# Kernel tuning notes

Measured on AMD Instinct MI355X. Metric: run time of the kernel, lower is better.

Reference implementation:

```python
import jax, jax.numpy as jnp
import numpy as np
import math

B, S, H, NH, DK, K = 256, 200, 768, 12, 64, 64
EPS = 1e-12

def setup_inputs() -> dict:
    key = jax.random.key(0)
    ks = jax.random.split(key, 8)
    sc = 0.02
    return {
        "x": jax.random.normal(ks[0], (B, S, H), dtype=jnp.float32),
        "mask": jnp.ones((B, 1, S), dtype=jnp.float32),
        "Wq": jax.random.normal(ks[1], (H, H), dtype=jnp.float32) * sc,
        "bq": jnp.zeros((H,), dtype=jnp.float32),
        "Wk": jax.random.normal(ks[2], (H, H), dtype=jnp.float32) * sc,
        "bk": jnp.zeros((H,), dtype=jnp.float32),
        "Wv": jax.random.normal(ks[3], (H, H), dtype=jnp.float32) * sc,
        "bv": jnp.zeros((H,), dtype=jnp.float32),
        "We": jax.random.normal(ks[4], (K, S), dtype=jnp.float32) * sc,
        "be": jnp.zeros((K,), dtype=jnp.float32),
        "Wf": jax.random.normal(ks[5], (K, S), dtype=jnp.float32) * sc,
        "bf": jnp.zeros((K,), dtype=jnp.float32),
        "Wd": jax.random.normal(ks[6], (H, H), dtype=jnp.float32) * sc,
        "bd": jnp.zeros((H,), dtype=jnp.float32),
        "gamma": jnp.ones((H,), dtype=jnp.float32),
        "beta": jnp.zeros((H,), dtype=jnp.float32),
    }

def _heads(t):  # [B,S,H] -> [B,NH,S,DK]
    return t.reshape(B, S, NH, DK).transpose(0, 2, 1, 3)

def reference(x, mask, Wq, bq, Wk, bk, Wv, bv, We, be, Wf, bf, Wd, bd, gamma, beta):
    q = _heads(x @ Wq.T + bq)
    k = _heads(x @ Wk.T + bk)
    v = _heads(x @ Wv.T + bv)
    m = mask[:, 0:1, :, None]            # [B,1,S,1]
    k = k * m
    v = v * m
    # Linformer seq projections: E on value, F on key (applied along seq axis)
    v = jnp.einsum("bhsd,ks->bhkd", v, We) + be[:, None]   # [B,NH,K,DK]
    k = jnp.einsum("bhsd,ks->bhkd", k, Wf) + bf[:, None]   # [B,NH,K,DK]
    scores = jnp.einsum("bhqd,bhkd->bhqk", q, k) / math.sqrt(DK)
    p_attn = jax.nn.softmax(scores, axis=-1)               # [B,NH,S,K]
    ctx = jnp.einsum("bhqk,bhkd->bhqd", p_attn, v)         # [B,NH,S,DK]
    ctx = ctx.transpose(0, 2, 1, 3).reshape(B, S, H)
    h = ctx @ Wd.T + bd + x                                # dense + residual (dropout=0)
    mu = jnp.mean(h, axis=-1, keepdims=True)
    var = jnp.mean(jnp.square(h - mu), axis=-1, keepdims=True)
    out = (h - mu) / jnp.sqrt(var + EPS) * gamma + beta
    return out, p_attn
```

## Files before the change

kernel.cpp:

```cpp
#include <hip/hip_runtime.h>
#include <stdint.h>

typedef unsigned short u16;
typedef short bf16x8 __attribute__((ext_vector_type(8)));
typedef float f32x4 __attribute__((ext_vector_type(4)));
typedef unsigned short u16x4 __attribute__((ext_vector_type(4)));

#define NB   256
#define NS   200
#define NHID 768
#define NHEAD 12
#define NDK  64
#define NK   64
#define NBH  (NB*NHEAD)
#define NM   (NB*NS)

__device__ __forceinline__ u16 f2b(float f){
  unsigned u = __builtin_bit_cast(unsigned, f);
  return (u16)((u + 0x7FFFu + ((u>>16)&1u)) >> 16);
}
__device__ __forceinline__ float b2f(u16 b){
  return __builtin_bit_cast(float, (unsigned)b << 16);
}
__device__ __forceinline__ bf16x8 pack8(const float* v){
  bf16x8 r;
#pragma unroll
  for (int i=0;i<8;i++) r[i] = (short)f2b(v[i]);
  return r;
}
__device__ __forceinline__ f32x4 mfma16(bf16x8 a, bf16x8 b, f32x4 c){
  return __builtin_amdgcn_mfma_f32_16x16x32_bf16(a, b, c, 0, 0, 0);
}
__device__ __forceinline__ void gload16(u16* l, const u16* g){
  __builtin_amdgcn_global_load_lds(
      (const __attribute__((address_space(1))) void*)g,
      (__attribute__((address_space(3))) void*)l, 16, 0, 0);
}

__global__ __launch_bounds__(256) void prep_kernel(
    const float* __restrict__ Wq, const float* __restrict__ Wk,
    const float* __restrict__ Wv, const float* __restrict__ Wd,
    const float* __restrict__ Wf, const float* __restrict__ We,
    const float* __restrict__ mask,
    u16* __restrict__ Wqb, u16* __restrict__ Wkb,
    u16* __restrict__ Wvb, u16* __restrict__ Wdb,
    u16* __restrict__ Wfeb, float* __restrict__ rs)
{
  const int blk = blockIdx.x, t = threadIdx.x;
  const int i = blk*256 + t;
  Wqb[i]=f2b(Wq[i]); Wkb[i]=f2b(Wk[i]); Wvb[i]=f2b(Wv[i]); Wdb[i]=f2b(Wd[i]);
  if (blk < 128){
    float v = 0.f;
    if (t < NS) v = (blk<64) ? Wf[blk*NS+t] : We[(blk-64)*NS+t];
    Wfeb[blk*256+t] = f2b(v);
  }
  if (blk >= 1024 && blk < 1280 && t < 128){
    const int b = blk-1024;
    const float* src = (t<64) ? (Wf + t*NS) : (We + (t-64)*NS);
    float acc = 0.f;
    for (int s=0;s<NS;s++) acc += src[s]*mask[b*NS+s];
    rs[b*128+t] = acc;
  }
}

__global__ __launch_bounds__(256) void gemm_yfe2(
    const float* __restrict__ x, const float* __restrict__ mask,
    const u16* __restrict__ Wfeb, u16* __restrict__ yfe,
    u16* __restrict__ xb)
{
  __shared__ u16 Al[128*64];
  __shared__ u16 Bl[128*72];
  __shared__ float Ml[256];
  const int t=threadIdx.x, w=t>>6, lane=t&63, hi=lane>>4, lo=lane&15;
  const int sr=lane>>3, sc=lane&7;
  const int b=blockIdx.x, col0=blockIdx.y*128;
  const int a16 = t&15, q4 = t>>4;
  const int ss0 = q4*4;
  const int swzw = (a16&7)<<3;

  Ml[t] = (t<NS) ? mask[b*NS+t] : 0.f;

  f32x4 acc[4][4];
#pragma unroll
  for(int i=0;i<4;i++)
#pragma unroll
    for(int j=0;j<4;j++) acc[i][j]=(f32x4)0.0f;

  const u16* Ab=&Al[((w>>1)*64+lo)*64 + hi*8];
  int nb_[4], sw_[4];
#pragma unroll
  for (int j=0;j<4;j++){
    const int n = (w&1)*64 + j*16 + lo;
    nb_[j] = n*72;
    sw_[j] = ((n>>3)&7)<<3;
  }
  __syncthreads();

  for (int kt=0; kt<256; kt+=64){
#pragma unroll
    for (int i8=0;i8<4;i8++){
      const int r = w*32 + i8*8 + sr;
      gload16(&Al[r*64 + sc*8], Wfeb + (size_t)r*256 + kt + sc*8);
    }
    float vv[4][8];
#pragma unroll
    for (int ii=0;ii<4;ii++){
      const int s = kt + ss0 + ii;
      const int srow = (s<NS) ? s : (NS-1);
      const float* gp = x + ((size_t)b*NS + srow)*NHID + col0 + a16*8;
      float4 u0 = *(const float4*)gp, u1 = *(const float4*)(gp+4);
      if (s < NS){
        float tu[8] = {u0.x,u0.y,u0.z,u0.w,u1.x,u1.y,u1.z,u1.w};
        *(bf16x8*)(xb + ((size_t)b*NS + s)*NHID + col0 + a16*8) = pack8(tu);
      }
      const float m = Ml[s];
      vv[ii][0]=u0.x*m; vv[ii][1]=u0.y*m; vv[ii][2]=u0.z*m; vv[ii][3]=u0.w*m;
      vv[ii][4]=u1.x*m; vv[ii][5]=u1.y*m; vv[ii][6]=u1.z*m; vv[ii][7]=u1.w*m;
    }
    const int ss_swz = ss0 ^ swzw;
#pragma unroll
    for (int h=0;h<8;h++){
      u16x4 p;
      p[0]=f2b(vv[0][h]); p[1]=f2b(vv[1][h]);
      p[2]=f2b(vv[2][h]); p[3]=f2b(vv[3][h]);
      *(u16x4*)&Bl[(a16*8+h)*72 + ss_swz] = p;
    }
    asm volatile("s_waitcnt vmcnt(0)" ::: "memory");
    __syncthreads();
#pragma unroll
    for (int ks=0; ks<2; ks++){
      bf16x8 a[4], bfr[4];
#pragma unroll
      for (int i=0;i<4;i++) a[i]   = *(const bf16x8*)(Ab + i*16*64 + ks*32);
#pragma unroll
      for (int j=0;j<4;j++){
        const int s8 = ks*32 + hi*8;
        bfr[j] = *(const bf16x8*)&Bl[nb_[j] + (s8 ^ sw_[j])];
      }
#pragma unroll
      for (int i=0;i<4;i++)
#pragma unroll
        for (int j=0;j<4;j++) acc[i][j] = mfma16(a[i], bfr[j], acc[i][j]);
    }
    __syncthreads();
  }
  const int mbase=(w>>1)*64, nbase=col0+(w&1)*64;
#pragma unroll
  for (int i=0;i<4;i++)
#pragma unroll
    for (int r=0;r<4;r++){
      const int m = mbase + i*16 + hi*4 + r;
#pragma unroll
      for (int j=0;j<4;j++){
        const int n = nbase + j*16 + lo;
        yfe[(size_t)b*98304 + (size_t)m*NHID + n] = f2b(acc[i][j][r]);
      }
    }
}

template<int EPI>
__global__ __launch_bounds__(512, 2) void gemm_ring(
    const u16* __restrict__ Ag_, const u16* __restrict__ Bg_,
    const float* __restrict__ bias, const u16* __restrict__ resid,
    u16* __restrict__ Cout)
{
  __shared__ u16 AS[4][8192];
  __shared__ u16 BS[4][8192];
  const int t = threadIdx.x;
  const int w = t>>6, lane = t&63, hi = lane>>4, lo = lane&15;
  const int wm = w>>2, wn = w&3;
  const int bid = blockIdx.x;
  const int row0 = ((bid/24)*8 + (bid&7))*256;
  const int col0 = ((bid>>3)%3)*256;
  const u16* Ag = Ag_ + (size_t)row0*NHID;
  const u16* Bg = Bg_ + (size_t)col0*NHID;
  const int rp0 = t>>3, cc = t&7;

  f32x4 acc[8][4];
#pragma unroll
  for (int i=0;i<8;i++)
#pragma unroll
    for (int j=0;j<4;j++) acc[i][j] = (f32x4)0.0f;

  int aoff[8], boff[4];
#pragma unroll
  for (int i=0;i<8;i++){
    const int r = wm*128 + i*16 + lo;
    const int rp = r>>1, c = (r&1)*4 + hi;
    aoff[i] = rp*64 + ((c ^ (rp&7))<<3);
  }
#pragma unroll
  for (int j=0;j<4;j++){
    const int n = wn*64 + j*16 + lo;
    const int rp = n>>1, c = (n&1)*4 + hi;
    boff[j] = rp*64 + ((c ^ (rp&7))<<3);
  }

  auto stage = [&](int s, int kt){
#pragma unroll
    for (int i8=0;i8<2;i8++){
      const int rp = i8*64 + rp0;
      const int c  = cc ^ (rp&7);
      const int grow = rp*2 + (c>>2);
      const int gcol = (c&3)<<3;
      gload16(&AS[s][rp*64 + cc*8], Ag + (size_t)grow*NHID + kt + gcol);
      gload16(&BS[s][rp*64 + cc*8], Bg + (size_t)grow*NHID + kt + gcol);
    }
  };
  auto body = [&](const u16* as_, const u16* bs_){
    bf16x8 av[8], bvv[4];
#pragma unroll
    for (int j=0;j<4;j++) bvv[j] = *(const bf16x8*)(bs_ + boff[j]);
#pragma unroll
    for (int i=0;i<8;i++) av[i] = *(const bf16x8*)(as_ + aoff[i]);
    __builtin_amdgcn_s_setprio(1);
#pragma unroll
    for (int i=0;i<8;i++)
#pragma unroll
      for (int j=0;j<4;j++) acc[i][j] = mfma16(av[i], bvv[j], acc[i][j]);
    __builtin_amdgcn_s_setprio(0);
  };
  auto step = [&](int tt, int s){
    if (tt+3 < 24) stage((s+3)&3, (tt+3)*32);
    body(AS[s], BS[s]);
    if (tt <= 20)      { asm volatile("s_waitcnt vmcnt(8)" ::: "memory"); }
    else if (tt == 21) { asm volatile("s_waitcnt vmcnt(4)" ::: "memory"); }
    else if (tt == 22) { asm volatile("s_waitcnt vmcnt(0)" ::: "memory"); }
    if (tt < 23){
      __builtin_amdgcn_sched_barrier(0);
      asm volatile("s_barrier" ::: "memory");
      __builtin_amdgcn_sched_barrier(0);
    }
  };

  stage(0,0); stage(1,32); stage(2,64);
  asm volatile("s_waitcnt vmcnt(8)" ::: "memory");
  asm volatile("s_barrier" ::: "memory");
  __builtin_amdgcn_sched_barrier(0);

#pragma unroll
  for (int tt=0; tt<24; tt+=4){
    step(tt,0); step(tt+1,1); step(tt+2,2); step(tt+3,3);
  }

#pragma unroll
  for (int i=0;i<8;i++)
#pragma unroll
    for (int q=0;q<4;q++){
      const int m = row0 + wm*128 + i*16 + hi*4 + q;
#pragma unroll
      for (int j=0;j<4;j++){
        const int n = col0 + wn*64 + j*16 + lo;
        float v = acc[i][j][q] + bias[n];
        if constexpr (EPI==0){
          const int b = m/NS, s = m - b*NS;
          Cout[(((size_t)b*NHEAD + (n>>6))*NS + s)*NDK + (n&63)] = f2b(v);
        } else {
          const size_t gi = (size_t)m*NHID + n;
          Cout[gi] = f2b(v + b2f(resid[gi]));
        }
      }
    }
}

__global__ __launch_bounds__(256) void gemm_projkv(
    const u16* __restrict__ yfe, const u16* __restrict__ Wkb,
    const u16* __restrict__ Wvb, const float* __restrict__ rs,
    const float* __restrict__ bk, const float* __restrict__ bv,
    const float* __restrict__ bff, const float* __restrict__ bee,
    u16* __restrict__ kproj, u16* __restrict__ vout)
{
  __shared__ u16 S[192*64];
  const int t=threadIdx.x, w=t>>6, lane=t&63, hi=lane>>4, lo=lane&15;
  const int sr=lane>>3, sc=lane&7;
  const int bid=blockIdx.x;
  const int b = (bid/96)*8 + (bid&7);
  const int jj = (bid>>3)%12;
  const int colb = jj%6, z = jj/6;

  if (z==0){
    u16* Al = S;
    u16* Bl = S + 64*64;
    const int col0=colb*128;
    const u16* yf = yfe + (size_t)b*98304;
    f32x4 acc[2][4];
#pragma unroll
    for(int i=0;i<2;i++)
#pragma unroll
      for(int j=0;j<4;j++) acc[i][j]=(f32x4)0.0f;
    const u16* Ab=&Al[((w>>1)*32+lo)*64 + hi*8];
    const u16* Bb=&Bl[((w&1)*64+lo)*64 + hi*8];
    for (int kt=0; kt<NHID; kt+=64){
#pragma unroll
      for (int i8=0;i8<2;i8++){
        const int r = w*16 + i8*8 + sr;
        gload16(&Al[r*64 + sc*8], yf + (size_t)r*NHID + kt + sc*8);
      }
#pragma unroll
      for (int i8=0;i8<4;i8++){
        const int r = w*32 + i8*8 + sr;
        gload16(&Bl[r*64 + sc*8], Wkb + (size_t)(col0+r)*NHID + kt + sc*8);
      }
      asm volatile("s_waitcnt vmcnt(0)" ::: "memory");
      __syncthreads();
#pragma unroll
      for (int ks=0; ks<2; ks++){
        bf16x8 a[2], bfr[4];
#pragma unroll
        for (int i=0;i<2;i++) a[i]   = *(const bf16x8*)(Ab + i*16*64 + ks*32);
#pragma unroll
        for (int j=0;j<4;j++) bfr[j] = *(const bf16x8*)(Bb + j*16*64 + ks*32);
#pragma unroll
        for (int i=0;i<2;i++)
#pragma unroll
          for (int j=0;j<4;j++) acc[i][j] = mfma16(a[i], bfr[j], acc[i][j]);
      }
      __syncthreads();
    }
    const int mbase=(w>>1)*32, nbase=col0+(w&1)*64;
#pragma unroll
    for (int i=0;i<2;i++)
#pragma unroll
      for (int r=0;r<4;r++){
        const int m = mbase + i*16 + hi*4 + r;
        const float rsv = rs[b*128 + m], bfv = bff[m];
#pragma unroll
        for (int j=0;j<4;j++){
          const int n = nbase + j*16 + lo;
          kproj[(size_t)b*49152 + (size_t)m*NHID + n] = f2b(acc[i][j][r] + rsv*bk[n] + bfv);
        }
      }
  } else {
    u16* Al = S;
    u16* Bl = S + 128*64;
    const int row0=colb*128;
    const u16* ye = yfe + (size_t)b*98304 + 49152;
    f32x4 acc[4][2];
#pragma unroll
    for(int i=0;i<4;i++)
#pragma unroll
      for(int j=0;j<2;j++) acc[i][j]=(f32x4)0.0f;
    const u16* Ab=&Al[((w>>1)*64+lo)*64 + hi*8];
    const u16* Bb=&Bl[((w&1)*32+lo)*64 + hi*8];
    for (int kt=0; kt<NHID; kt+=64){
#pragma unroll
      for (int i8=0;i8<4;i8++){
        const int r = w*32 + i8*8 + sr;
        gload16(&Al[r*64 + sc*8], Wvb + (size_t)(row0+r)*NHID + kt + sc*8);
      }
#pragma unroll
      for (int i8=0;i8<2;i8++){
        const int r = w*16 + i8*8 + sr;
        gload16(&Bl[r*64 + sc*8], ye + (size_t)r*NHID + kt + sc*8);
      }
      asm volatile("s_waitcnt vmcnt(0)" ::: "memory");
      __syncthreads();
#pragma unroll
      for (int ks=0; ks<2; ks++){
        bf16x8 a[4], bfr[2];
#pragma unroll
        for (int i=0;i<4;i++) a[i]   = *(const bf16x8*)(Ab + i*16*64 + ks*32);
#pragma unroll
        for (int j=0;j<2;j++) bfr[j] = *(const bf16x8*)(Bb + j*16*64 + ks*32);
#pragma unroll
        for (int i=0;i<4;i++)
#pragma unroll
          for (int j=0;j<2;j++) acc[i][j] = mfma16(a[i], bfr[j], acc[i][j]);
      }
      __syncthreads();
    }
    const int mbase=row0+(w>>1)*64, nbase=(w&1)*32;
#pragma unroll
    for (int i=0;i<4;i++)
#pragma unroll
      for (int r=0;r<4;r++){
        const int m = mbase + i*16 + hi*4 + r;
        const float bvv = bv[m];
#pragma unroll
        for (int j=0;j<2;j++){
          const int n = nbase + j*16 + lo;
          vout[(size_t)b*49152 + (size_t)m*64 + n] = f2b(acc[i][j][r] + rs[b*128+64+n]*bvv + bee[n]);
        }
      }
  }
}

__global__ __launch_bounds__(256) void attn_kernel(
    const u16* __restrict__ qb,
    const u16* __restrict__ kproj,
    const u16* __restrict__ vprojT,
    float* __restrict__ pout,
    u16* __restrict__ ctxb)
{
  __shared__ u16 QL[208*72];
  __shared__ u16 KP[64*72];
  __shared__ u16 VP[64*72];
  const int t=threadIdx.x, w=t>>6, lane=t&63, hi=lane>>4, lo=lane&15;
  const int bh = blockIdx.x, b=bh/NHEAD, hh=bh%NHEAD;
  for (int c=t;c<1600;c+=256){
    const int row=c>>3, col8=(c&7)*8;
    *(bf16x8*)&QL[row*72+col8] = *(const bf16x8*)(qb + (size_t)bh*12800 + c*8);
  }
  if (t<72){ const int row=200+t/9, col8=(t%9)*8; *(bf16x8*)&QL[row*72+col8]=(bf16x8)0; }
  for (int c=t;c<512;c+=256){
    const int row=c>>3, col8=(c&7)*8;
    *(bf16x8*)&KP[row*72+col8] = *(const bf16x8*)(kproj  + (size_t)b*49152 + (size_t)row*NHID + hh*64 + col8);
    *(bf16x8*)&VP[row*72+col8] = *(const bf16x8*)(vprojT + (size_t)b*49152 + (size_t)(hh*64+row)*64 + col8);
  }
  __syncthreads();
  const int mf0 = (w==0)?0:(1+w*3);
  const int nmf = (w==0)?4:3;
  f32x4 acc[4][4];
#pragma unroll
  for(int i=0;i<4;i++)
#pragma unroll
    for(int j=0;j<4;j++) acc[i][j]=(f32x4)0.0f;
#pragma unroll
  for (int ks=0; ks<2; ks++){
    bf16x8 a[4], bb[4];
#pragma unroll
    for (int j=0;j<4;j++) bb[j]=*(const bf16x8*)&KP[(j*16+lo)*72 + ks*32 + hi*8];
#pragma unroll
    for (int i=0;i<4;i++) if (i<nmf) a[i]=*(const bf16x8*)&QL[((mf0+i)*16+lo)*72 + ks*32 + hi*8];
#pragma unroll
    for (int i=0;i<4;i++) if (i<nmf)
#pragma unroll
      for (int j=0;j<4;j++)
        acc[i][j]=mfma16(a[i],bb[j],acc[i][j]);
  }
  __syncthreads();

#pragma unroll
  for (int i=0;i<4;i++) if (i<nmf){
#pragma unroll
    for (int r=0;r<4;r++){
      const int q = (mf0+i)*16 + hi*4 + r;
      float s0=acc[i][0][r]*0.125f, s1=acc[i][1][r]*0.125f,
            s2=acc[i][2][r]*0.125f, s3=acc[i][3][r]*0.125f;
      float mx=fmaxf(fmaxf(s0,s1),fmaxf(s2,s3));
      mx=fmaxf(mx,__shfl_xor(mx,1)); mx=fmaxf(mx,__shfl_xor(mx,2));
      mx=fmaxf(mx,__shfl_xor(mx,4)); mx=fmaxf(mx,__shfl_xor(mx,8));
      float e0=__expf(s0-mx), e1=__expf(s1-mx), e2=__expf(s2-mx), e3=__expf(s3-mx);
      float sm=e0+e1+e2+e3;
      sm+=__shfl_xor(sm,1); sm+=__shfl_xor(sm,2); sm+=__shfl_xor(sm,4); sm+=__shfl_xor(sm,8);
      const float inv=1.0f/sm;
      const float p0=e0*inv,p1=e1*inv,p2=e2*inv,p3=e3*inv;
      if (q<NS){
        float* pg = pout + ((size_t)bh*NS + q)*NK + lo;
        pg[0]=p0; pg[16]=p1; pg[32]=p2; pg[48]=p3;
      }
      u16* pl = &QL[q*72 + lo];
      pl[0]=f2b(p0); pl[16]=f2b(p1); pl[32]=f2b(p2); pl[48]=f2b(p3);
    }
  }
  f32x4 acc2[4][4];
#pragma unroll
  for(int i=0;i<4;i++)
#pragma unroll
    for(int j=0;j<4;j++) acc2[i][j]=(f32x4)0.0f;
#pragma unroll
  for (int ks=0; ks<2; ks++){
    bf16x8 a[4], bb[4];
#pragma unroll
    for (int j=0;j<4;j++) bb[j]=*(const bf16x8*)&VP[(j*16+lo)*72 + ks*32 + hi*8];
#pragma unroll
    for (int i=0;i<4;i++) if (i<nmf) a[i]=*(const bf16x8*)&QL[((mf0+i)*16+lo)*72 + ks*32 + hi*8];
#pragma unroll
    for (int i=0;i<4;i++) if (i<nmf)
#pragma unroll
      for (int j=0;j<4;j++)
        acc2[i][j]=mfma16(a[i],bb[j],acc2[i][j]);
  }
#pragma unroll
  for (int i=0;i<4;i++) if (i<nmf)
#pragma unroll
    for (int r=0;r<4;r++){
      const int q=(mf0+i)*16+hi*4+r;
      if (q<NS){
#pragma unroll
        for (int j=0;j<4;j++){
          const int d=j*16+lo;
          ctxb[((size_t)b*NS+q)*NHID + hh*NDK + d] = f2b(acc2[i][j][r]);
        }
      }
    }
}

__global__ __launch_bounds__(256) void ln2_kernel(
    const u16* __restrict__ h, const float* __restrict__ gamma,
    const float* __restrict__ beta, float* __restrict__ outp)
{
  const int t = threadIdx.x, wid = t>>6, lane = t&63;
  float g_[12], be_[12];
#pragma unroll
  for (int k=0;k<3;k++){
    float4 gg = *(const float4*)(gamma + lane*12 + k*4);
    float4 bb = *(const float4*)(beta  + lane*12 + k*4);
    g_[k*4+0]=gg.x; g_[k*4+1]=gg.y; g_[k*4+2]=gg.z; g_[k*4+3]=gg.w;
    be_[k*4+0]=bb.x; be_[k*4+1]=bb.y; be_[k*4+2]=bb.z; be_[k*4+3]=bb.w;
  }
  for (int row = blockIdx.x*4 + wid; row < NM; row += 1600*4){
    const u16* hr = h + (size_t)row*NHID + lane*12;
    u16x4 a0 = *(const u16x4*)hr;
    u16x4 a1 = *(const u16x4*)(hr+4);
    u16x4 a2 = *(const u16x4*)(hr+8);
    float v[12];
#pragma unroll
    for (int k=0;k<4;k++){
      v[k]   = b2f(a0[k]);
      v[4+k] = b2f(a1[k]);
      v[8+k] = b2f(a2[k]);
    }
    float s=0.f, q=0.f;
#pragma unroll
    for (int k=0;k<12;k++){ s+=v[k]; q+=v[k]*v[k]; }
#pragma unroll
    for (int m=1;m<64;m<<=1){ s+=__shfl_xor(s,m); q+=__shfl_xor(q,m); }
    const float mu = s*(1.0f/768.0f);
    const float rsv = rsqrtf(q*(1.0f/768.0f) - mu*mu + 1e-12f);
    float* orow = outp + (size_t)row*NHID + lane*12;
#pragma unroll
    for (int k=0;k<12;k++) orow[k] = (v[k]-mu)*rsv*g_[k] + be_[k];
  }
}

extern "C" void kernel_launch(void* const* d_in, const int* in_sizes, int n_in,
                              void* d_out, int out_size, void* d_ws, size_t ws_size,
                              hipStream_t stream)
{
  (void)in_sizes; (void)n_in; (void)out_size; (void)ws_size;
  const float* x    = (const float*)d_in[0];
  const float* mask = (const float*)d_in[1];
  const float* Wq   = (const float*)d_in[2];
  const float* bq   = (const float*)d_in[3];
  const float* Wk   = (const float*)d_in[4];
  const float* bk   = (const float*)d_in[5];
  const float* Wv   = (const float*)d_in[6];
  const float* bv   = (const float*)d_in[7];
  const float* We   = (const float*)d_in[8];
  const float* be   = (const float*)d_in[9];
  const float* Wf   = (const float*)d_in[10];
  const float* bf   = (const float*)d_in[11];
  const float* Wd   = (const float*)d_in[12];
  const float* bd   = (const float*)d_in[13];
  const float* gamma= (const float*)d_in[14];
  const float* beta = (const float*)d_in[15];

  float* out  = (float*)d_out;
  float* pout = out + (size_t)NM*NHID;

  char* ws = (char*)d_ws;
  u16* xb    = (u16*)(ws);
  u16* qb    = (u16*)(ws + 78643200ull);
  u16* yfe   = (u16*)(ws + 166723584ull);
  u16* kproj = (u16*)(ws + 217055232ull);
  u16* Wqb   = (u16*)(ws + 242221056ull);
  u16* Wkb   = (u16*)(ws + 243400704ull);
  u16* Wvb   = (u16*)(ws + 244580352ull);
  u16* Wdb   = (u16*)(ws + 245760000ull);
  u16* Wfeb  = (u16*)(ws + 246939648ull);
  float* rsb = (float*)(ws + 247005184ull);
  u16* vprojT= (u16*)(ws + 247136256ull);
  u16* ctxb  = (u16*)(ws + 272302080ull);
  u16* hb    = (u16*)(ws + 350945280ull);

  prep_kernel<<<2304,256,0,stream>>>(Wq,Wk,Wv,Wd,Wf,We,mask,Wqb,Wkb,Wvb,Wdb,Wfeb,rsb);
  gemm_yfe2<<<dim3(NB,6),256,0,stream>>>(x,mask,Wfeb,yfe,xb);
  gemm_ring<0><<<600,512,0,stream>>>(xb,Wqb,bq,nullptr,qb);
  gemm_projkv<<<3072,256,0,stream>>>(yfe,Wkb,Wvb,rsb,bk,bv,bf,be,kproj,vprojT);
  attn_kernel<<<NBH,256,0,stream>>>(qb,kproj,vprojT,pout,ctxb);
  gemm_ring<1><<<600,512,0,stream>>>(ctxb,Wdb,bd,xb,hb);
  ln2_kernel<<<1600,256,0,stream>>>(hb,gamma,beta,out);
}
```

Before: 511.1 us.

## Fuse Q projection GEMM into attention kernel, dropping the separate Q pass

```diff
diff --git a/kernel.cpp b/kernel.cpp
--- a/kernel.cpp
+++ b/kernel.cpp
@@ -158,7 +158,6 @@
     }
 }
 
-template<int EPI>
 __global__ __launch_bounds__(512, 2) void gemm_ring(
     const u16* __restrict__ Ag_, const u16* __restrict__ Bg_,
     const float* __restrict__ bias, const u16* __restrict__ resid,
@@ -251,14 +250,8 @@
 #pragma unroll
       for (int j=0;j<4;j++){
         const int n = col0 + wn*64 + j*16 + lo;
-        float v = acc[i][j][q] + bias[n];
-        if constexpr (EPI==0){
-          const int b = m/NS, s = m - b*NS;
-          Cout[(((size_t)b*NHEAD + (n>>6))*NS + s)*NDK + (n&63)] = f2b(v);
-        } else {
-          const size_t gi = (size_t)m*NHID + n;
-          Cout[gi] = f2b(v + b2f(resid[gi]));
-        }
+        const size_t gi = (size_t)m*NHID + n;
+        Cout[gi] = f2b(acc[i][j][q] + bias[n] + b2f(resid[gi]));
       }
     }
 }
@@ -385,32 +378,81 @@
   }
 }
 
-__global__ __launch_bounds__(256) void attn_kernel(
-    const u16* __restrict__ qb,
+__global__ __launch_bounds__(256) void attn2_kernel(
+    const u16* __restrict__ xb,
+    const u16* __restrict__ Wqb,
+    const float* __restrict__ bq,
     const u16* __restrict__ kproj,
     const u16* __restrict__ vprojT,
     float* __restrict__ pout,
     u16* __restrict__ ctxb)
 {
-  __shared__ u16 QL[208*72];
-  __shared__ u16 KP[64*72];
-  __shared__ u16 VP[64*72];
+  __shared__ u16 SH[25856];
+  u16* QL = SH;
+  u16* XA = SH + 14976;
+  u16* WB = SH + 23296;
+  u16* KP = SH + 14976;
+  u16* VP = SH + 19584;
   const int t=threadIdx.x, w=t>>6, lane=t&63, hi=lane>>4, lo=lane&15;
-  const int bh = blockIdx.x, b=bh/NHEAD, hh=bh%NHEAD;
-  for (int c=t;c<1600;c+=256){
-    const int row=c>>3, col8=(c&7)*8;
-    *(bf16x8*)&QL[row*72+col8] = *(const bf16x8*)(qb + (size_t)bh*12800 + c*8);
-  }
-  if (t<72){ const int row=200+t/9, col8=(t%9)*8; *(bf16x8*)&QL[row*72+col8]=(bf16x8)0; }
+  const int bid=blockIdx.x;
+  const int b  = (bid/96)*8 + (bid&7);
+  const int hh = (bid>>3)%12;
+  const int bh = b*NHEAD + hh;
+  const int mf0 = (w==0)?0:(1+w*3);
+  const int nmf = (w==0)?4:3;
+
+  f32x4 acc[4][4];
+#pragma unroll
+  for(int i=0;i<4;i++)
+#pragma unroll
+    for(int j=0;j<4;j++) acc[i][j]=(f32x4)0.0f;
+
+  for (int kt=0; kt<NHID; kt+=32){
+    for (int c=t; c<832; c+=256){
+      const int row=c>>2, col8=(c&3)*8;
+      const int srow = (row<NS) ? row : (NS-1);
+      *(bf16x8*)&XA[row*40+col8] =
+        *(const bf16x8*)(xb + ((size_t)b*NS+srow)*NHID + kt + col8);
+    }
+    {
+      const int row=t>>2, col8=(t&3)*8;
+      *(bf16x8*)&WB[row*40+col8] =
+        *(const bf16x8*)(Wqb + (size_t)(hh*64+row)*NHID + kt + col8);
+    }
+    __syncthreads();
+    bf16x8 a[4], bbf[4];
+#pragma unroll
+    for (int j=0;j<4;j++) bbf[j] = *(const bf16x8*)&WB[(j*16+lo)*40 + hi*8];
+#pragma unroll
+    for (int i=0;i<4;i++) if (i<nmf) a[i] = *(const bf16x8*)&XA[((mf0+i)*16+lo)*40 + hi*8];
+#pragma unroll
+    for (int i=0;i<4;i++) if (i<nmf)
+#pragma unroll
+      for (int j=0;j<4;j++) acc[i][j] = mfma16(a[i], bbf[j], acc[i][j]);
+    __syncthreads();
+  }
+  {
+    float bq_[4];
+#pragma unroll
+    for (int j=0;j<4;j++) bq_[j] = bq[hh*64 + j*16 + lo];
+#pragma unroll
+    for (int i=0;i<4;i++) if (i<nmf)
+#pragma unroll
+      for (int r=0;r<4;r++){
+        const int q = (mf0+i)*16 + hi*4 + r;
+#pragma unroll
+        for (int j=0;j<4;j++)
+          QL[q*72 + j*16 + lo] = f2b(acc[i][j][r] + bq_[j]);
+      }
+  }
+  __syncthreads();
   for (int c=t;c<512;c+=256){
     const int row=c>>3, col8=(c&7)*8;
     *(bf16x8*)&KP[row*72+col8] = *(const bf16x8*)(kproj  + (size_t)b*49152 + (size_t)row*NHID + hh*64 + col8);
     *(bf16x8*)&VP[row*72+col8] = *(const bf16x8*)(vprojT + (size_t)b*49152 + (size_t)(hh*64+row)*64 + col8);
   }
   __syncthreads();
-  const int mf0 = (w==0)?0:(1+w*3);
-  const int nmf = (w==0)?4:3;
-  f32x4 acc[4][4];
+
 #pragma unroll
   for(int i=0;i<4;i++)
 #pragma unroll
@@ -551,7 +593,6 @@
 
   char* ws = (char*)d_ws;
   u16* xb    = (u16*)(ws);
-  u16* qb    = (u16*)(ws + 78643200ull);
   u16* yfe   = (u16*)(ws + 166723584ull);
   u16* kproj = (u16*)(ws + 217055232ull);
   u16* Wqb   = (u16*)(ws + 242221056ull);
@@ -566,9 +607,8 @@
 
   prep_kernel<<<2304,256,0,stream>>>(Wq,Wk,Wv,Wd,Wf,We,mask,Wqb,Wkb,Wvb,Wdb,Wfeb,rsb);
   gemm_yfe2<<<dim3(NB,6),256,0,stream>>>(x,mask,Wfeb,yfe,xb);
-  gemm_ring<0><<<600,512,0,stream>>>(xb,Wqb,bq,nullptr,qb);
   gemm_projkv<<<3072,256,0,stream>>>(yfe,Wkb,Wvb,rsb,bk,bv,bf,be,kproj,vprojT);
-  attn_kernel<<<NBH,256,0,stream>>>(qb,kproj,vprojT,pout,ctxb);
-  gemm_ring<1><<<600,512,0,stream>>>(ctxb,Wdb,bd,xb,hb);
+  attn2_kernel<<<3072,256,0,stream>>>(xb,Wqb,bq,kproj,vprojT,pout,ctxb);
+  gemm_ring<<<600,512,0,stream>>>(ctxb,Wdb,bd,xb,hb);
   ln2_kernel<<<1600,256,0,stream>>>(hb,gamma,beta,out);
 }
```

After: 670.6 us. 1.31x slower.
